# Performance work log

Hardware: AMD Instinct MI355X
Metric: run time of the kernel (lower is better)

## Reference

```python
import jax, jax.numpy as jnp
import numpy as np

MAX_MARKER = 16


def setup_inputs() -> dict:
    key = jax.random.key(0)
    ks = jax.random.split(key, 7)
    B, W, H = 65536, 512, 8
    s1 = 1.0 / np.sqrt(W)
    s2 = 1.0 / np.sqrt(H)
    return {
        "x": jax.random.normal(ks[0], (B, W), dtype=jnp.float32),
        "W1": jax.random.uniform(ks[1], (H, W), jnp.float32, -s1, s1),
        "b1": jax.random.uniform(ks[2], (H,), jnp.float32, -s1, s1),
        "W2": jax.random.uniform(ks[3], (H, H), jnp.float32, -s2, s2),
        "b2": jax.random.uniform(ks[4], (H,), jnp.float32, -s2, s2),
        "W3": jax.random.uniform(ks[5], (W, H), jnp.float32, -s2, s2),
        "b3": jax.random.uniform(ks[6], (W,), jnp.float32, -s2, s2),
    }


def reference(x, W1, b1, W2, b2, W3, b3):
    # tiny MLP: window -> 8 -> 8 -> window
    h = jax.nn.relu(x @ W1.T + b1)
    h = jax.nn.relu(h @ W2.T + b2)
    y = h @ W3.T + b3
    p = jax.nn.softmax(y, axis=1)
    # force endpoints on (x.data[:,0]=1; x.data[:,-1]=1)
    p = p.at[:, 0].set(1.0).at[:, -1].set(1.0)
    # top-k along dim 1; threshold = min of the top-k values per row
    top_vals, _ = jax.lax.top_k(p, MAX_MARKER)
    thr = top_vals[:, -1:]  # sorted desc -> last is min, shape [B,1]
    # binary mask writes: >= thr -> 1, else 0
    return jnp.where(p >= thr, 1.0, 0.0).astype(p.dtype)
```

## Files before the change

### kernel.cpp

```cpp
#include <hip/hip_runtime.h>
#include <math.h>

#define B_ROWS 65536
#define WDIM 512
#define HDIM 8
#define THREADS 512

typedef float native_float4 __attribute__((ext_vector_type(4)));

template<int CTRL, int ROWM>
__device__ __forceinline__ float dpp_mov(float oldv, float x) {
    return __int_as_float(__builtin_amdgcn_update_dpp(
        __float_as_int(oldv), __float_as_int(x), CTRL, ROWM, 0xF, false));
}

__device__ __forceinline__ float wave_sum(float x) {
    x += dpp_mov<0x121, 0xF>(0.f, x);
    x += dpp_mov<0x122, 0xF>(0.f, x);
    x += dpp_mov<0x124, 0xF>(0.f, x);
    x += dpp_mov<0x128, 0xF>(0.f, x);
    x += dpp_mov<0x142, 0xA>(0.f, x);
    x += dpp_mov<0x143, 0xC>(0.f, x);
    return __int_as_float(__builtin_amdgcn_readlane(__float_as_int(x), 63));
}

__device__ __forceinline__ float dot8(native_float4 a0, native_float4 a1,
                                      native_float4 b0, native_float4 b1) {
    float s = a0.x * b0.x;
    s = fmaf(a0.y, b0.y, s); s = fmaf(a0.z, b0.z, s); s = fmaf(a0.w, b0.w, s);
    s = fmaf(a1.x, b1.x, s); s = fmaf(a1.y, b1.y, s);
    s = fmaf(a1.z, b1.z, s); s = fmaf(a1.w, b1.w, s);
    return s;
}

__device__ __forceinline__ unsigned ford(float f) {
    unsigned b = __float_as_uint(f);
    return b ^ ((unsigned)((int)b >> 31) | 0x80000000u);
}

__global__ __launch_bounds__(THREADS, 2)
void fused_mlp_topk(const float* __restrict__ x,
                    const float* __restrict__ W1,
                    const float* __restrict__ b1,
                    const float* __restrict__ W2,
                    const float* __restrict__ b2,
                    const float* __restrict__ W3,
                    const float* __restrict__ b3,
                    float* __restrict__ out)
{
    __shared__ __align__(16) float sW1[HDIM * WDIM];
    __shared__ __align__(16) float sW3t[HDIM * WDIM];
    __shared__ __align__(16) float sb3[WDIM];

    const int tid = threadIdx.x;
    for (int i = tid; i < HDIM * WDIM; i += THREADS) sW1[i] = W1[i];
    for (int i = tid; i < HDIM * WDIM; i += THREADS) {
        int r = i >> 3, k = i & 7;
        sW3t[k * WDIM + r] = W3[i];
    }
    for (int i = tid; i < WDIM; i += THREADS) sb3[i] = b3[i];
    __syncthreads();

    const int lane = tid & 63;
    const int wave_id = blockIdx.x * (THREADS / 64) + (tid >> 6);

    const native_float4* sW1v = reinterpret_cast<const native_float4*>(sW1);
    const native_float4* sW3v = reinterpret_cast<const native_float4*>(sW3t);
    const native_float4* sb3v = reinterpret_cast<const native_float4*>(sb3);

    int ra = wave_id * 2;
    const native_float4* xpa = reinterpret_cast<const native_float4*>(x + (size_t)ra * WDIM);
    const native_float4* xpb = xpa + (WDIM / 4);
    native_float4 xa0 = __builtin_nontemporal_load(xpa + lane);
    native_float4 xa1 = __builtin_nontemporal_load(xpa + lane + 64);
    native_float4 xb0 = __builtin_nontemporal_load(xpb + lane);
    native_float4 xb1 = __builtin_nontemporal_load(xpb + lane + 64);

    #pragma unroll 1
    for (int it = 0; it < 4; ++it) {
        float pa[HDIM], pb[HDIM];
        #pragma unroll
        for (int j = 0; j < HDIM; ++j) {
            native_float4 w0 = sW1v[j * 128 + lane];
            native_float4 w1 = sW1v[j * 128 + lane + 64];
            pa[j] = dot8(xa0, xa1, w0, w1);
            pb[j] = dot8(xb0, xb1, w0, w1);
        }
        float h1a[HDIM], h1b[HDIM];
        #pragma unroll
        for (int j = 0; j < HDIM; ++j) {
            float sa = wave_sum(pa[j]) + b1[j];
            float sb = wave_sum(pb[j]) + b1[j];
            h1a[j] = sa > 0.f ? sa : 0.f;
            h1b[j] = sb > 0.f ? sb : 0.f;
        }

        float h2a[HDIM], h2b[HDIM];
        #pragma unroll
        for (int j = 0; j < HDIM; ++j) {
            float va = b2[j], vb = b2[j];
            #pragma unroll
            for (int k = 0; k < HDIM; ++k) {
                const float w = W2[j * HDIM + k];
                va = fmaf(w, h1a[k], va);
                vb = fmaf(w, h1b[k], vb);
            }
            h2a[j] = va > 0.f ? va : 0.f;
            h2b[j] = vb > 0.f ? vb : 0.f;
        }

        native_float4 ya0 = sb3v[lane];
        native_float4 ya1 = sb3v[lane + 64];
        native_float4 yb0 = ya0, yb1 = ya1;
        #pragma unroll
        for (int k = 0; k < HDIM; ++k) {
            const float ha = h2a[k], hb = h2b[k];
            native_float4 w0 = sW3v[k * 128 + lane];
            native_float4 w1 = sW3v[k * 128 + lane + 64];
            ya0 += ha * w0;  ya1 += ha * w1;
            yb0 += hb * w0;  yb1 += hb * w1;
        }

        const int nra = ra + 16384;
        native_float4 nxa0, nxa1, nxb0, nxb1;
        if (it < 3) {
            const native_float4* nxpa = reinterpret_cast<const native_float4*>(x + (size_t)nra * WDIM);
            const native_float4* nxpb = nxpa + (WDIM / 4);
            nxa0 = __builtin_nontemporal_load(nxpa + lane);
            nxa1 = __builtin_nontemporal_load(nxpa + lane + 64);
            nxb0 = __builtin_nontemporal_load(nxpb + lane);
            nxb1 = __builtin_nontemporal_load(nxpb + lane + 64);
        }

        unsigned ua[8], ub[8];
        ua[0] = ford(ya0.x); ua[1] = ford(ya0.y); ua[2] = ford(ya0.z); ua[3] = ford(ya0.w);
        ua[4] = ford(ya1.x); ua[5] = ford(ya1.y); ua[6] = ford(ya1.z); ua[7] = ford(ya1.w);
        ub[0] = ford(yb0.x); ub[1] = ford(yb0.y); ub[2] = ford(yb0.z); ub[3] = ford(yb0.w);
        ub[4] = ford(yb1.x); ub[5] = ford(yb1.y); ub[6] = ford(yb1.z); ub[7] = ford(yb1.w);
        if (lane == 0)  { ua[0] = 0u; ub[0] = 0u; }
        if (lane == 63) { ua[7] = 0u; ub[7] = 0u; }

        unsigned Ua = 0u, Ub = 0u;
        unsigned tha = 0u, thb = 0u;
        #pragma unroll 1
        for (int b = 31; b >= 0; --b) {
            const unsigned bit = 1u << b;
            if (!tha) {
                const unsigned cf = Ua | bit;
                int ca = 0;
                #pragma unroll
                for (int t = 0; t < 8; ++t)
                    ca += __popcll(__ballot(ua[t] > cf));
                if (ca == 14)      tha = cf + 1u;
                else if (ca > 14)  Ua = cf;
            }
            if (!thb) {
                const unsigned cf = Ub | bit;
                int cb = 0;
                #pragma unroll
                for (int t = 0; t < 8; ++t)
                    cb += __popcll(__ballot(ub[t] > cf));
                if (cb == 14)      thb = cf + 1u;
                else if (cb > 14)  Ub = cf;
            }
            if (tha && thb) break;
        }
        if (!tha) tha = Ua + 1u;
        if (!thb) thb = Ub + 1u;

        native_float4 r0, r1, q0, q1;
        r0.x = ua[0] >= tha ? 1.f : 0.f;  r0.y = ua[1] >= tha ? 1.f : 0.f;
        r0.z = ua[2] >= tha ? 1.f : 0.f;  r0.w = ua[3] >= tha ? 1.f : 0.f;
        r1.x = ua[4] >= tha ? 1.f : 0.f;  r1.y = ua[5] >= tha ? 1.f : 0.f;
        r1.z = ua[6] >= tha ? 1.f : 0.f;  r1.w = ua[7] >= tha ? 1.f : 0.f;
        q0.x = ub[0] >= thb ? 1.f : 0.f;  q0.y = ub[1] >= thb ? 1.f : 0.f;
        q0.z = ub[2] >= thb ? 1.f : 0.f;  q0.w = ub[3] >= thb ? 1.f : 0.f;
        q1.x = ub[4] >= thb ? 1.f : 0.f;  q1.y = ub[5] >= thb ? 1.f : 0.f;
        q1.z = ub[6] >= thb ? 1.f : 0.f;  q1.w = ub[7] >= thb ? 1.f : 0.f;
        if (lane == 0)  { r0.x = 1.f; q0.x = 1.f; }
        if (lane == 63) { r1.w = 1.f; q1.w = 1.f; }

        native_float4* oa = reinterpret_cast<native_float4*>(out + (size_t)ra * WDIM);
        native_float4* ob = oa + (WDIM / 4);
        __builtin_nontemporal_store(r0, oa + lane);
        __builtin_nontemporal_store(r1, oa + lane + 64);
        __builtin_nontemporal_store(q0, ob + lane);
        __builtin_nontemporal_store(q1, ob + lane + 64);

        ra = nra;
        xa0 = nxa0; xa1 = nxa1; xb0 = nxb0; xb1 = nxb1;
    }
}

extern "C" void kernel_launch(void* const* d_in, const int* in_sizes, int n_in,
                              void* d_out, int out_size, void* d_ws, size_t ws_size,
                              hipStream_t stream) {
    const float* x  = (const float*)d_in[0];
    const float* W1 = (const float*)d_in[1];
    const float* b1 = (const float*)d_in[2];
    const float* W2 = (const float*)d_in[3];
    const float* b2 = (const float*)d_in[4];
    const float* W3 = (const float*)d_in[5];
    const float* b3 = (const float*)d_in[6];
    float* out = (float*)d_out;

    fused_mlp_topk<<<dim3(1024), dim3(THREADS), 0, stream>>>(x, W1, b1, W2, b2, W3, b3, out);
}
```

Baseline: 326.3 us.

## Software-pipeline next-iteration W1 dot products into top-k bit search

Result: slower. 338.6 us (+3.7%).

```diff
diff --git a/kernel.cpp b/kernel.cpp
--- a/kernel.cpp
+++ b/kernel.cpp
@@ -69,16 +69,14 @@
     const native_float4* sb3v = reinterpret_cast<const native_float4*>(sb3);
 
     int ra = wave_id * 2;
-    const native_float4* xpa = reinterpret_cast<const native_float4*>(x + (size_t)ra * WDIM);
-    const native_float4* xpb = xpa + (WDIM / 4);
-    native_float4 xa0 = __builtin_nontemporal_load(xpa + lane);
-    native_float4 xa1 = __builtin_nontemporal_load(xpa + lane + 64);
-    native_float4 xb0 = __builtin_nontemporal_load(xpb + lane);
-    native_float4 xb1 = __builtin_nontemporal_load(xpb + lane + 64);
-
-    #pragma unroll 1
-    for (int it = 0; it < 4; ++it) {
-        float pa[HDIM], pb[HDIM];
+    float pa[HDIM], pb[HDIM];
+    {
+        const native_float4* xpa = reinterpret_cast<const native_float4*>(x + (size_t)ra * WDIM);
+        const native_float4* xpb = xpa + (WDIM / 4);
+        native_float4 xa0 = __builtin_nontemporal_load(xpa + lane);
+        native_float4 xa1 = __builtin_nontemporal_load(xpa + lane + 64);
+        native_float4 xb0 = __builtin_nontemporal_load(xpb + lane);
+        native_float4 xb1 = __builtin_nontemporal_load(xpb + lane + 64);
         #pragma unroll
         for (int j = 0; j < HDIM; ++j) {
             native_float4 w0 = sW1v[j * 128 + lane];
@@ -86,6 +84,19 @@
             pa[j] = dot8(xa0, xa1, w0, w1);
             pb[j] = dot8(xb0, xb1, w0, w1);
         }
+    }
+
+    #pragma unroll 1
+    for (int it = 0; it < 4; ++it) {
+        const int nra = ra + 16384;
+        const size_t safe_row = (it < 3) ? (size_t)nra : 0;
+        const native_float4* nxpa = reinterpret_cast<const native_float4*>(x + safe_row * WDIM);
+        const native_float4* nxpb = nxpa + (WDIM / 4);
+        native_float4 nxa0 = __builtin_nontemporal_load(nxpa + lane);
+        native_float4 nxa1 = __builtin_nontemporal_load(nxpa + lane + 64);
+        native_float4 nxb0 = __builtin_nontemporal_load(nxpb + lane);
+        native_float4 nxb1 = __builtin_nontemporal_load(nxpb + lane + 64);
+
         float h1a[HDIM], h1b[HDIM];
         #pragma unroll
         for (int j = 0; j < HDIM; ++j) {
@@ -121,17 +132,6 @@
             yb0 += hb * w0;  yb1 += hb * w1;
         }
 
-        const int nra = ra + 16384;
-        native_float4 nxa0, nxa1, nxb0, nxb1;
-        if (it < 3) {
-            const native_float4* nxpa = reinterpret_cast<const native_float4*>(x + (size_t)nra * WDIM);
-            const native_float4* nxpb = nxpa + (WDIM / 4);
-            nxa0 = __builtin_nontemporal_load(nxpa + lane);
-            nxa1 = __builtin_nontemporal_load(nxpa + lane + 64);
-            nxb0 = __builtin_nontemporal_load(nxpb + lane);
-            nxb1 = __builtin_nontemporal_load(nxpb + lane + 64);
-        }
-
         unsigned ua[8], ub[8];
         ua[0] = ford(ya0.x); ua[1] = ford(ya0.y); ua[2] = ford(ya0.z); ua[3] = ford(ya0.w);
         ua[4] = ford(ya1.x); ua[5] = ford(ya1.y); ua[6] = ford(ya1.z); ua[7] = ford(ya1.w);
@@ -142,8 +142,38 @@
 
         unsigned Ua = 0u, Ub = 0u;
         unsigned tha = 0u, thb = 0u;
+
+        float npa[HDIM], npb[HDIM];
+        #pragma unroll
+        for (int b = 31; b >= 24; --b) {
+            const int j = 31 - b;
+            native_float4 w0 = sW1v[j * 128 + lane];
+            native_float4 w1 = sW1v[j * 128 + lane + 64];
+            const unsigned bit = 1u << b;
+            if (!tha) {
+                const unsigned cf = Ua | bit;
+                int ca = 0;
+                #pragma unroll
+                for (int t = 0; t < 8; ++t)
+                    ca += __popcll(__ballot(ua[t] > cf));
+                if (ca == 14)      tha = cf + 1u;
+                else if (ca > 14)  Ua = cf;
+            }
+            if (!thb) {
+                const unsigned cf = Ub | bit;
+                int cb = 0;
+                #pragma unroll
+                for (int t = 0; t < 8; ++t)
+                    cb += __popcll(__ballot(ub[t] > cf));
+                if (cb == 14)      thb = cf + 1u;
+                else if (cb > 14)  Ub = cf;
+            }
+            npa[j] = dot8(nxa0, nxa1, w0, w1);
+            npb[j] = dot8(nxb0, nxb1, w0, w1);
+        }
+
         #pragma unroll 1
-        for (int b = 31; b >= 0; --b) {
+        for (int b = 23; b >= 0; --b) {
             const unsigned bit = 1u << b;
             if (!tha) {
                 const unsigned cf = Ua | bit;
@@ -188,7 +218,8 @@
         __builtin_nontemporal_store(q1, ob + lane + 64);
 
         ra = nra;
-        xa0 = nxa0; xa1 = nxa1; xb0 = nxb0; xb1 = nxb1;
+        #pragma unroll
+        for (int j = 0; j < HDIM; ++j) { pa[j] = npa[j]; pb[j] = npb[j]; }
     }
 }
 
```
